# Kernel tuning notes

Measured on AMD Instinct MI355X. Metric: run time of the kernel, lower is better.

## Reference

```python
import jax, jax.numpy as jnp
import numpy as np

N_HEAD = 16
N_EMBD = 2048


def _rope(x):
    # x: (B, H, L, D). FAITHFUL to source: _apply_rope unpacks (B, L, H, D) on a
    # (B, H, L, D) tensor, so rotation angle = head_index * inv_freq, broadcast over
    # all sequence positions (a latent bug in the original, reproduced exactly).
    B, H, L, D = x.shape
    inv_freq = 1.0 / (10000.0 ** (jnp.arange(0, D, 2, dtype=jnp.float32) / D))  # (D/2,)
    theta = jnp.arange(H, dtype=jnp.float32)[:, None] * inv_freq[None, :]       # (H, D/2)
    cos = jnp.cos(theta)[None, :, None, :]  # (1, H, 1, D/2)
    sin = jnp.sin(theta)[None, :, None, :]
    xp = x.astype(jnp.float32).reshape(B, H, L, D // 2, 2)
    x0, x1 = xp[..., 0], xp[..., 1]
    r0 = x0 * cos - x1 * sin
    r1 = x0 * sin + x1 * cos
    return jnp.stack([r0, r1], axis=-1).reshape(B, H, L, D).astype(x.dtype)


def setup_inputs() -> dict:
    key = jax.random.key(0)
    k1, k2, k3 = jax.random.split(key, 3)
    B, L, C = 2, 2048, N_EMBD
    s = 1.0 / np.sqrt(C).astype(np.float32)
    x = jax.random.normal(k1, (B, L, C), dtype=jnp.float32)
    w_attn = jax.random.normal(k2, (3 * C, C), dtype=jnp.float32) * s
    w_proj = jax.random.normal(k3, (C, C), dtype=jnp.float32) * s
    return {"x": x, "w_attn": w_attn, "w_proj": w_proj}


def reference(x, w_attn, w_proj):
    B, L, C = x.shape
    H = N_HEAD
    D = C // H
    qkv = x @ w_attn.T                       # (B, L, 3C)
    q, k, v = jnp.split(qkv, 3, axis=2)
    q = q.reshape(B, L, H, D).transpose(0, 2, 1, 3)  # (B, H, L, D)
    k = k.reshape(B, L, H, D).transpose(0, 2, 1, 3)
    v = v.reshape(B, L, H, D).transpose(0, 2, 1, 3)
    q = _rope(q)
    k = _rope(k)
    attn = jnp.einsum('bhqd,bhkd->bhqk', q, k) * (1.0 / np.sqrt(D).astype(np.float32))
    causal = jnp.tril(jnp.ones((L, L), dtype=bool))
    attn = jnp.where(causal[None, None], attn, -jnp.inf)
    attn = jax.nn.softmax(attn, axis=-1)
    y = jnp.einsum('bhqk,bhkd->bhqd', attn, v)
    y = y.transpose(0, 2, 1, 3).reshape(B, L, C)
    return y @ w_proj.T
```

## Files before the change

kernel.cpp:

```cpp
#include <hip/hip_runtime.h>

typedef __attribute__((ext_vector_type(8))) short bf16x8;
typedef __attribute__((ext_vector_type(4))) float f32x4;

__device__ __forceinline__ unsigned short f2bf(float f) {
  unsigned int u = __float_as_uint(f);
  u += 0x7FFF + ((u >> 16) & 1);
  return (unsigned short)(u >> 16);
}

__device__ __forceinline__ void gload_lds16(const void* g, void* l) {
  __builtin_amdgcn_global_load_lds(
      (const __attribute__((address_space(1))) unsigned int*)g,
      (__attribute__((address_space(3))) unsigned int*)l,
      16, 0, 0);
}

#define MF(a, b, c) __builtin_amdgcn_mfma_f32_16x16x32_bf16((a), (b), (c), 0, 0, 0)
#define FENCE asm volatile("" ::: "memory")

__global__ void cast_f32_to_bf16(const float* __restrict__ in,
                                 unsigned short* __restrict__ out, int n4) {
  int stride = gridDim.x * blockDim.x;
  for (int i = blockIdx.x * blockDim.x + threadIdx.x; i < n4; i += stride) {
    float4 v = ((const float4*)in)[i];
    ushort4 o;
    o.x = f2bf(v.x); o.y = f2bf(v.y); o.z = f2bf(v.z); o.w = f2bf(v.w);
    ((ushort4*)out)[i] = o;
  }
}

template<int EPI>
__global__ __launch_bounds__(512, 2)
void gemm8p(const unsigned short* __restrict__ A,
            const unsigned short* __restrict__ Bw,
            float* __restrict__ Cf,
            unsigned short* __restrict__ Qo,
            unsigned short* __restrict__ Ko,
            unsigned short* __restrict__ Vo,
            int M, int N, int K, int Lseq) {
  __shared__ unsigned short lds[2][2][2][8192];
  const int tid = threadIdx.x;
  const int lane = tid & 63, w = tid >> 6;
  const int wm = w >> 2, wn = w & 3;
  const int bh = wn >> 1;
  const int bcol = (wn & 1) * 64;
  const int g4 = lane >> 4, r16 = lane & 15;
  const long arow0 = (long)blockIdx.y * 256;
  const long brow0 = (long)blockIdx.x * 256;

#define LDA(db, mf, kk)                                                       \
  (*(const bf16x8*)((const char*)&lds[0][db][wm][0] +                         \
                    (((mf)*16 + r16) << 7) +                                  \
                    ((((kk)*4 + g4) ^ (r16 & 7)) << 4)))
#define LDB(db, nf, kk)                                                       \
  (*(const bf16x8*)((const char*)&lds[1][db][bh][0] +                         \
                    ((bcol + (nf)*16 + r16) << 7) +                           \
                    ((((kk)*4 + g4) ^ (r16 & 7)) << 4)))

#define STG(mat, db, half, kt)                                                \
  do {                                                                        \
    const unsigned short* g_ = (mat) ? Bw : A;                                \
    long r0_ = ((mat) ? brow0 : arow0) + (half)*128;                          \
    int k0_ = (kt) << 6;                                                      \
    _Pragma("unroll")                                                         \
    for (int c_ = 0; c_ < 2; ++c_) {                                          \
      int off_ = (c_ << 13) + (tid << 4);                                     \
      int row_ = off_ >> 7;                                                   \
      int scb_ = ((off_ >> 4) & 7) ^ (row_ & 7);                              \
      gload_lds16(g_ + (r0_ + row_) * (long)K + k0_ + scb_ * 8,               \
                  (char*)&lds[mat][db][half][0] + off_);                      \
    }                                                                         \
  } while (0)

  f32x4 acc[8][4];
#pragma unroll
  for (int i = 0; i < 8; ++i)
#pragma unroll
    for (int j = 0; j < 4; ++j) acc[i][j] = (f32x4){0.f, 0.f, 0.f, 0.f};

  bf16x8 b00, b01, b10, b11, b20, b21, b30, b31;

#define PH(db, q, STAGE_STMT, VMSTMT)                                         \
  do {                                                                        \
    bf16x8 a00 = LDA(db, 2*(q), 0), a01 = LDA(db, 2*(q), 1);                  \
    bf16x8 a10 = LDA(db, 2*(q)+1, 0), a11 = LDA(db, 2*(q)+1, 1);              \
    STAGE_STMT;                                                               \
    VMSTMT;                                                                   \
    FENCE; __builtin_amdgcn_s_barrier(); FENCE;                               \
    __builtin_amdgcn_s_setprio(1);                                            \
    acc[2*(q)][0] = MF(a00, b00, acc[2*(q)][0]);                              \
    acc[2*(q)][0] = MF(a01, b01, acc[2*(q)][0]);                              \
    acc[2*(q)][1] = MF(a00, b10, acc[2*(q)][1]);                              \
    acc[2*(q)][1] = MF(a01, b11, acc[2*(q)][1]);                              \
    acc[2*(q)][2] = MF(a00, b20, acc[2*(q)][2]);                              \
    acc[2*(q)][2] = MF(a01, b21, acc[2*(q)][2]);                              \
    acc[2*(q)][3] = MF(a00, b30, acc[2*(q)][3]);                              \
    acc[2*(q)][3] = MF(a01, b31, acc[2*(q)][3]);                              \
    acc[2*(q)+1][0] = MF(a10, b00, acc[2*(q)+1][0]);                          \
    acc[2*(q)+1][0] = MF(a11, b01, acc[2*(q)+1][0]);                          \
    acc[2*(q)+1][1] = MF(a10, b10, acc[2*(q)+1][1]);                          \
    acc[2*(q)+1][1] = MF(a11, b11, acc[2*(q)+1][1]);                          \
    acc[2*(q)+1][2] = MF(a10, b20, acc[2*(q)+1][2]);                          \
    acc[2*(q)+1][2] = MF(a11, b21, acc[2*(q)+1][2]);                          \
    acc[2*(q)+1][3] = MF(a10, b30, acc[2*(q)+1][3]);                          \
    acc[2*(q)+1][3] = MF(a11, b31, acc[2*(q)+1][3]);                          \
    __builtin_amdgcn_s_setprio(0);                                            \
    FENCE; __builtin_amdgcn_s_barrier(); FENCE;                               \
  } while (0)

#define LOADB(db)                                                             \
  do {                                                                        \
    b00 = LDB(db, 0, 0); b01 = LDB(db, 0, 1);                                 \
    b10 = LDB(db, 1, 0); b11 = LDB(db, 1, 1);                                 \
    b20 = LDB(db, 2, 0); b21 = LDB(db, 2, 1);                                 \
    b30 = LDB(db, 3, 0); b31 = LDB(db, 3, 1);                                 \
  } while (0)

#define VM4 asm volatile("s_waitcnt vmcnt(4)" ::: "memory")

  const int NT = K >> 6;
  STG(0, 0, 0, 0); STG(0, 0, 1, 0);
  STG(1, 0, 0, 0); STG(1, 0, 1, 0);
  STG(1, 1, 0, 1); STG(1, 1, 1, 1);
  VM4;
  FENCE; __builtin_amdgcn_s_barrier(); FENCE;

  for (int i = 0; i < (NT >> 1); ++i) {
    const int t1 = 2 * i + 1;
    int n0 = 2 * i + 2; if (n0 > NT - 1) n0 = NT - 1;
    int n1 = 2 * i + 3; if (n1 > NT - 1) n1 = NT - 1;
    LOADB(0);
    PH(0, 0, STG(0, 1, 0, t1), );
    PH(0, 1, STG(0, 1, 1, t1), );
    PH(0, 2, STG(1, 0, 0, n0), );
    PH(0, 3, STG(1, 0, 1, n0), VM4);
    LOADB(1);
    PH(1, 0, STG(0, 0, 0, n0), );
    PH(1, 1, STG(0, 0, 1, n0), );
    PH(1, 2, STG(1, 1, 0, n1), );
    PH(1, 3, STG(1, 1, 1, n1), VM4);
  }
  asm volatile("s_waitcnt vmcnt(0)" ::: "memory");

  const float qscale = 0.08838834764831845f;
#pragma unroll
  for (int mf = 0; mf < 8; ++mf) {
#pragma unroll
    for (int nf = 0; nf < 4; ++nf) {
#pragma unroll
      for (int i = 0; i < 4; ++i) {
        long row = arow0 + wm * 128 + mf * 16 + 4 * g4 + i;
        long col = brow0 + wn * 64 + nf * 16 + r16;
        float v = acc[mf][nf][i];
        if (EPI == 0) {
          Cf[row * N + col] = v;
        } else {
          int which = (int)(col >> 11);
          int h = ((int)col >> 7) & 15;
          int d = (int)col & 127;
          int b = (int)(row >> 11);
          int l = (int)row & 2047;
          long bhead = (long)(b * 16 + h);
          if (which == 0)
            Qo[(bhead * Lseq + l) * 128 + d] = f2bf(v * qscale);
          else if (which == 1)
            Ko[(bhead * Lseq + l) * 128 + d] = f2bf(v);
          else
            Vo[(bhead * 128 + d) * Lseq + l] = f2bf(v);
        }
      }
    }
  }
#undef LDA
#undef LDB
#undef STG
#undef PH
#undef LOADB
#undef VM4
}

template<int EPI>
__global__ __launch_bounds__(256, 4)
void gemm_bt(const unsigned short* __restrict__ A,
             const unsigned short* __restrict__ Bw,
             float* __restrict__ Cf,
             unsigned short* __restrict__ Qo,
             unsigned short* __restrict__ Ko,
             unsigned short* __restrict__ Vo,
             int M, int N, int K, int Lseq, int nbx) {
  __shared__ unsigned short As[2][128 * 32];
  __shared__ unsigned short Bs[2][128 * 32];
  const int tid = threadIdx.x;
  const int lane = tid & 63, w = tid >> 6;
  const int wm = w >> 1, wn = w & 1;
  const int g4 = lane >> 4, r16 = lane & 15;

  const int nwg = gridDim.x;
  const int cpx = nwg >> 3;
  const int bid = (blockIdx.x & 7) * cpx + (blockIdx.x >> 3);
  const long arow0 = (long)(bid / nbx) * 128;
  const long brow0 = (long)(bid % nbx) * 128;

#define STAGE_G(k0_, buf_)                                                    \
  do {                                                                        \
    _Pragma("unroll")                                                         \
    for (int c_ = 0; c_ < 2; ++c_) {                                          \
      int off_ = (w << 11) + (c_ << 10) + (lane << 4);                        \
      int row_ = off_ >> 6;                                                   \
      int cbs_ = ((off_ >> 4) & 3) ^ ((row_ >> 1) & 3);                       \
      gload_lds16(A + (arow0 + row_) * (long)K + (k0_) + cbs_ * 8,            \
                  (char*)As[buf_] + off_);                                    \
      gload_lds16(Bw + (brow0 + row_) * (long)K + (k0_) + cbs_ * 8,           \
                  (char*)Bs[buf_] + off_);                                    \
    }                                                                         \
  } while (0)

  f32x4 acc[4][4];
#pragma unroll
  for (int i = 0; i < 4; ++i)
#pragma unroll
    for (int j = 0; j < 4; ++j) acc[i][j] = (f32x4){0.f, 0.f, 0.f, 0.f};

  const int T = K >> 5;
  int cur = 0;
  STAGE_G(0, 0);

  for (int t = 0; t < T; ++t) {
    if (t < T - 1) {
      STAGE_G((t + 1) << 5, cur ^ 1);
      asm volatile("s_waitcnt vmcnt(4)" ::: "memory");
    } else {
      asm volatile("s_waitcnt vmcnt(0)" ::: "memory");
    }
    __builtin_amdgcn_s_barrier();

    const int rb = g4 ^ ((r16 >> 1) & 3);
    bf16x8 af[4], bf[4];
#pragma unroll
    for (int mf = 0; mf < 4; ++mf)
      af[mf] = *(const bf16x8*)((const char*)As[cur] +
                                ((64 * wm + 16 * mf + r16) << 6) + (rb << 4));
#pragma unroll
    for (int nf = 0; nf < 4; ++nf)
      bf[nf] = *(const bf16x8*)((const char*)Bs[cur] +
                                ((64 * wn + 16 * nf + r16) << 6) + (rb << 4));
#pragma unroll
    for (int mf = 0; mf < 4; ++mf)
#pragma unroll
      for (int nf = 0; nf < 4; ++nf)
        acc[mf][nf] = MF(af[mf], bf[nf], acc[mf][nf]);
    asm volatile("" ::: "memory");
    __builtin_amdgcn_s_barrier();
    cur ^= 1;
  }
#undef STAGE_G

  const float qscale = 0.08838834764831845f;
#pragma unroll
  for (int mf = 0; mf < 4; ++mf) {
#pragma unroll
    for (int nf = 0; nf < 4; ++nf) {
#pragma unroll
      for (int i = 0; i < 4; ++i) {
        long row = arow0 + 64 * wm + 16 * mf + 4 * g4 + i;
        long col = brow0 + 64 * wn + 16 * nf + r16;
        float v = acc[mf][nf][i];
        if (EPI == 0) {
          Cf[row * N + col] = v;
        } else {
          int which = (int)(col >> 11);
          int h = ((int)col >> 7) & 15;
          int d = (int)col & 127;
          int b = (int)(row >> 11);
          int l = (int)row & 2047;
          long bhead = (long)(b * 16 + h);
          if (which == 0)
            Qo[(bhead * Lseq + l) * 128 + d] = f2bf(v * qscale);
          else if (which == 1)
            Ko[(bhead * Lseq + l) * 128 + d] = f2bf(v);
          else
            Vo[(bhead * 128 + d) * Lseq + l] = f2bf(v);
        }
      }
    }
  }
}

__global__ __launch_bounds__(256, 2)
void attn_fwd(const unsigned short* __restrict__ Q,
              const unsigned short* __restrict__ K,
              const unsigned short* __restrict__ Vt,
              unsigned short* __restrict__ Y, int L) {
  const int D = 128;
  const int id = blockIdx.x;
  const int g = id & 7, kk = id >> 3;
  const int bh = (g << 2) + (kk >> 5);
  const int qt = 31 - (kk & 31);
  const int tid = threadIdx.x, lane = tid & 63, w = tid >> 6;
  const int g4 = lane >> 4, r16 = lane & 15;
  const int q0 = qt * 64;

  __shared__ unsigned short Klds[2 * 64 * 128];
  __shared__ unsigned short Vlds[2 * 128 * 64];
  __shared__ unsigned short P[4][16][72];

  const unsigned short* Qh = Q + (long)bh * L * D;
  const unsigned short* Kh = K + (long)bh * L * D;
  const unsigned short* Vh = Vt + (long)bh * D * L;

#define STAGE_TILE(kt_, buf_)                                                 \
  do {                                                                        \
    const int kbase_ = (kt_) * 64;                                            \
    _Pragma("unroll")                                                         \
    for (int r_ = 0; r_ < 4; ++r_) {                                          \
      int off_ = (tid << 4) + (r_ << 12);                                     \
      int krow_ = off_ >> 8, kcb_ = (off_ >> 4) & 15;                         \
      int kcbs_ = kcb_ ^ (krow_ & 7);                                         \
      gload_lds16(Kh + (long)(kbase_ + krow_) * 128 + kcbs_ * 8,              \
                  (char*)Klds + (buf_)*16384 + (w << 10) + (r_ << 12));       \
      int vrow_ = off_ >> 7, vcb_ = (off_ >> 4) & 7;                          \
      int vcbs_ = vcb_ ^ (vrow_ & 7);                                         \
      gload_lds16(Vh + (long)vrow_ * L + kbase_ + vcbs_ * 8,                  \
                  (char*)Vlds + (buf_)*16384 + (w << 10) + (r_ << 12));       \
    }                                                                         \
  } while (0)

  bf16x8 qf[4];
  {
    long qrow = q0 + 16 * w + r16;
#pragma unroll
    for (int ks = 0; ks < 4; ++ks)
      qf[ks] = *(const bf16x8*)(Qh + qrow * D + ks * 32 + g4 * 8);
  }
  f32x4 o[8];
#pragma unroll
  for (int j = 0; j < 8; ++j) o[j] = (f32x4){0.f, 0.f, 0.f, 0.f};
  float mrun[4] = {-1e30f, -1e30f, -1e30f, -1e30f};
  float lrun[4] = {0.f, 0.f, 0.f, 0.f};

  int cur = 0;
  STAGE_TILE(0, 0);

  for (int kt = 0; kt <= qt; ++kt) {
    if (kt < qt) {
      STAGE_TILE(kt + 1, cur ^ 1);
      asm volatile("s_waitcnt vmcnt(8)" ::: "memory");
    } else {
      asm volatile("s_waitcnt vmcnt(0)" ::: "memory");
    }
    __builtin_amdgcn_s_barrier();

    const char* Kl = (const char*)Klds + cur * 16384;
    const char* Vl = (const char*)Vlds + cur * 16384;

    f32x4 s[4];
#pragma unroll
    for (int nf = 0; nf < 4; ++nf) s[nf] = (f32x4){0.f, 0.f, 0.f, 0.f};
#pragma unroll
    for (int ks = 0; ks < 4; ++ks) {
#pragma unroll
      for (int nf = 0; nf < 4; ++nf) {
        int row = 16 * nf + r16;
        bf16x8 kf = *(const bf16x8*)(Kl + row * 256 +
                                     (((ks * 4 + g4) ^ (row & 7)) << 4));
        s[nf] = MF(qf[ks], kf, s[nf]);
      }
    }

    const bool diag = (kt == qt);
#pragma unroll
    for (int i = 0; i < 4; ++i) {
      int qg = q0 + 16 * w + 4 * g4 + i;
      float sv[4];
      float rmax = -1e30f;
#pragma unroll
      for (int nf = 0; nf < 4; ++nf) {
        float t = s[nf][i];
        if (diag && (kt * 64 + 16 * nf + r16) > qg) t = -1e30f;
        sv[nf] = t;
        rmax = fmaxf(rmax, t);
      }
      rmax = fmaxf(rmax, __shfl_xor(rmax, 1));
      rmax = fmaxf(rmax, __shfl_xor(rmax, 2));
      rmax = fmaxf(rmax, __shfl_xor(rmax, 4));
      rmax = fmaxf(rmax, __shfl_xor(rmax, 8));
      float mnew = fmaxf(mrun[i], rmax);
      float corr = __expf(mrun[i] - mnew);
      mrun[i] = mnew;
      float rs = 0.f;
#pragma unroll
      for (int nf = 0; nf < 4; ++nf) {
        float pv = __expf(sv[nf] - mnew);
        P[w][4 * g4 + i][16 * nf + r16] = f2bf(pv);
        rs += pv;
      }
      rs += __shfl_xor(rs, 1);
      rs += __shfl_xor(rs, 2);
      rs += __shfl_xor(rs, 4);
      rs += __shfl_xor(rs, 8);
      lrun[i] = lrun[i] * corr + rs;
#pragma unroll
      for (int nf2 = 0; nf2 < 8; ++nf2) o[nf2][i] *= corr;
    }
#pragma unroll
    for (int ks2 = 0; ks2 < 2; ++ks2) {
      bf16x8 pf = *(const bf16x8*)(&P[w][r16][ks2 * 32 + g4 * 8]);
#pragma unroll
      for (int nf2 = 0; nf2 < 8; ++nf2) {
        int row = 16 * nf2 + r16;
        bf16x8 vf = *(const bf16x8*)(Vl + row * 128 +
                                     (((ks2 * 4 + g4) ^ (row & 7)) << 4));
        o[nf2] = MF(pf, vf, o[nf2]);
      }
    }
    asm volatile("" ::: "memory");
    __builtin_amdgcn_s_barrier();
    cur ^= 1;
  }
#undef STAGE_TILE

  const int b = bh >> 4, h = bh & 15;
#pragma unroll
  for (int nf2 = 0; nf2 < 8; ++nf2) {
#pragma unroll
    for (int i = 0; i < 4; ++i) {
      long row = (long)b * L + q0 + 16 * w + 4 * g4 + i;
      float v = o[nf2][i] / lrun[i];
      Y[row * 2048 + h * 128 + 16 * nf2 + r16] = f2bf(v);
    }
  }
}

extern "C" void kernel_launch(void* const* d_in, const int* in_sizes, int n_in,
                              void* d_out, int out_size, void* d_ws,
                              size_t ws_size, hipStream_t stream) {
  const float* x = (const float*)d_in[0];
  const float* wa = (const float*)d_in[1];
  const float* wp = (const float*)d_in[2];
  float* out = (float*)d_out;
  const int B = 2, L = 2048, C = 2048;
  const int M = B * L;

  unsigned short* xb = (unsigned short*)d_ws;
  unsigned short* wab = xb + (size_t)M * C;
  unsigned short* wpb = wab + (size_t)3 * C * C;
  unsigned short* Qb = wpb + (size_t)C * C;
  unsigned short* Kb = Qb + (size_t)M * C;
  unsigned short* Vb = Kb + (size_t)M * C;
  unsigned short* Yb = Vb + (size_t)M * C;

  cast_f32_to_bf16<<<2048, 256, 0, stream>>>(x, xb, M * C / 4);
  cast_f32_to_bf16<<<2048, 256, 0, stream>>>(wa, wab, 3 * C * C / 4);
  cast_f32_to_bf16<<<1024, 256, 0, stream>>>(wp, wpb, C * C / 4);

  gemm8p<1><<<dim3(3 * C / 256, M / 256), 512, 0, stream>>>(
      xb, wab, nullptr, Qb, Kb, Vb, M, 3 * C, C, L);

  attn_fwd<<<1024, 256, 0, stream>>>(Qb, Kb, Vb, Yb, L);

  gemm_bt<0><<<(M / 128) * (C / 128), 256, 0, stream>>>(
      Yb, wpb, out, nullptr, nullptr, nullptr, M, C, C, L, C / 128);
}
```

Before: 332.8 us.

## Software-pipeline A-fragment LDS reads and swizzle block order in QKV GEMM

Restructures the QKV projection GEMM main loop so the A fragments for the next compute phase are read from LDS into registers (double-buffered aaA/aaB) while the current phase's MFMAs run. This removes one barrier per phase, cutting from two to one. It also changes the launch to a 1D grid of 384 blocks with a remapping that groups blocks sharing the same B (weight) tiles, aiming for better L2 reuse. The cost is more register pressure from the extra fragment buffers, and a reordered global-to-LDS staging schedule with vmcnt(2) waits that must stay race-free.

```diff
diff --git a/kernel.cpp b/kernel.cpp
--- a/kernel.cpp
+++ b/kernel.cpp
@@ -18,6 +18,7 @@
 
 #define MF(a, b, c) __builtin_amdgcn_mfma_f32_16x16x32_bf16((a), (b), (c), 0, 0, 0)
 #define FENCE asm volatile("" ::: "memory")
+#define BARF do { FENCE; __builtin_amdgcn_s_barrier(); FENCE; } while (0)
 
 __global__ void cast_f32_to_bf16(const float* __restrict__ in,
                                  unsigned short* __restrict__ out, int n4) {
@@ -39,74 +40,59 @@
             unsigned short* __restrict__ Ko,
             unsigned short* __restrict__ Vo,
             int M, int N, int K, int Lseq) {
-  __shared__ unsigned short lds[2][2][2][8192];
+  __shared__ unsigned short Al[2][2][8192];
+  __shared__ unsigned short Bl[2][2][8192];
   const int tid = threadIdx.x;
   const int lane = tid & 63, w = tid >> 6;
   const int wm = w >> 2, wn = w & 3;
   const int bh = wn >> 1;
   const int bcol = (wn & 1) * 64;
   const int g4 = lane >> 4, r16 = lane & 15;
-  const long arow0 = (long)blockIdx.y * 256;
-  const long brow0 = (long)blockIdx.x * 256;
+
+  const int swz = (blockIdx.x & 7) * 48 + (blockIdx.x >> 3);
+  const int bx = swz >> 4, by = swz & 15;
+  const long arow0 = (long)by * 256;
+  const long brow0 = (long)bx * 256;
 
 #define LDA(db, mf, kk)                                                       \
-  (*(const bf16x8*)((const char*)&lds[0][db][wm][0] +                         \
-                    (((mf)*16 + r16) << 7) +                                  \
+  (*(const bf16x8*)((const char*)&Al[db][wm][0] + (((mf)*16 + r16) << 7) +    \
                     ((((kk)*4 + g4) ^ (r16 & 7)) << 4)))
 #define LDB(db, nf, kk)                                                       \
-  (*(const bf16x8*)((const char*)&lds[1][db][bh][0] +                         \
+  (*(const bf16x8*)((const char*)&Bl[db][bh][0] +                             \
                     ((bcol + (nf)*16 + r16) << 7) +                           \
                     ((((kk)*4 + g4) ^ (r16 & 7)) << 4)))
 
-#define STG(mat, db, half, kt)                                                \
-  do {                                                                        \
-    const unsigned short* g_ = (mat) ? Bw : A;                                \
-    long r0_ = ((mat) ? brow0 : arow0) + (half)*128;                          \
+#define STGA(db, half, kt)                                                    \
+  do {                                                                        \
+    long r0_ = arow0 + (half)*128;                                            \
     int k0_ = (kt) << 6;                                                      \
     _Pragma("unroll")                                                         \
     for (int c_ = 0; c_ < 2; ++c_) {                                          \
       int off_ = (c_ << 13) + (tid << 4);                                     \
       int row_ = off_ >> 7;                                                   \
       int scb_ = ((off_ >> 4) & 7) ^ (row_ & 7);                              \
-      gload_lds16(g_ + (r0_ + row_) * (long)K + k0_ + scb_ * 8,               \
-                  (char*)&lds[mat][db][half][0] + off_);                      \
+      gload_lds16(A + (r0_ + row_) * (long)K + k0_ + scb_ * 8,                \
+                  (char*)&Al[db][half][0] + off_);                            \
     }                                                                         \
   } while (0)
-
-  f32x4 acc[8][4];
-#pragma unroll
-  for (int i = 0; i < 8; ++i)
-#pragma unroll
-    for (int j = 0; j < 4; ++j) acc[i][j] = (f32x4){0.f, 0.f, 0.f, 0.f};
-
-  bf16x8 b00, b01, b10, b11, b20, b21, b30, b31;
-
-#define PH(db, q, STAGE_STMT, VMSTMT)                                         \
-  do {                                                                        \
-    bf16x8 a00 = LDA(db, 2*(q), 0), a01 = LDA(db, 2*(q), 1);                  \
-    bf16x8 a10 = LDA(db, 2*(q)+1, 0), a11 = LDA(db, 2*(q)+1, 1);              \
-    STAGE_STMT;                                                               \
-    VMSTMT;                                                                   \
-    FENCE; __builtin_amdgcn_s_barrier(); FENCE;                               \
-    __builtin_amdgcn_s_setprio(1);                                            \
-    acc[2*(q)][0] = MF(a00, b00, acc[2*(q)][0]);                              \
-    acc[2*(q)][0] = MF(a01, b01, acc[2*(q)][0]);                              \
-    acc[2*(q)][1] = MF(a00, b10, acc[2*(q)][1]);                              \
-    acc[2*(q)][1] = MF(a01, b11, acc[2*(q)][1]);                              \
-    acc[2*(q)][2] = MF(a00, b20, acc[2*(q)][2]);                              \
-    acc[2*(q)][2] = MF(a01, b21, acc[2*(q)][2]);                              \
-    acc[2*(q)][3] = MF(a00, b30, acc[2*(q)][3]);                              \
-    acc[2*(q)][3] = MF(a01, b31, acc[2*(q)][3]);                              \
-    acc[2*(q)+1][0] = MF(a10, b00, acc[2*(q)+1][0]);                          \
-    acc[2*(q)+1][0] = MF(a11, b01, acc[2*(q)+1][0]);                          \
-    acc[2*(q)+1][1] = MF(a10, b10, acc[2*(q)+1][1]);                          \
-    acc[2*(q)+1][1] = MF(a11, b11, acc[2*(q)+1][1]);                          \
-    acc[2*(q)+1][2] = MF(a10, b20, acc[2*(q)+1][2]);                          \
-    acc[2*(q)+1][2] = MF(a11, b21, acc[2*(q)+1][2]);                          \
-    acc[2*(q)+1][3] = MF(a10, b30, acc[2*(q)+1][3]);                          \
-    acc[2*(q)+1][3] = MF(a11, b31, acc[2*(q)+1][3]);                          \
-    __builtin_amdgcn_s_setprio(0);                                            \
-    FENCE; __builtin_amdgcn_s_barrier(); FENCE;                               \
+#define STGB(db, half, kt)                                                    \
+  do {                                                                        \
+    long r0_ = brow0 + (half)*128;                                            \
+    int k0_ = (kt) << 6;                                                      \
+    _Pragma("unroll")                                                         \
+    for (int c_ = 0; c_ < 2; ++c_) {                                          \
+      int off_ = (c_ << 13) + (tid << 4);                                     \
+      int row_ = off_ >> 7;                                                   \
+      int scb_ = ((off_ >> 4) & 7) ^ (row_ & 7);                              \
+      gload_lds16(Bw + (r0_ + row_) * (long)K + k0_ + scb_ * 8,               \
+                  (char*)&Bl[db][half][0] + off_);                            \
+    }                                                                         \
+  } while (0)
+
+#define PREF(dst, db, q)                                                      \
+  do {                                                                        \
+    dst[0] = LDA(db, 2*(q), 0);   dst[1] = LDA(db, 2*(q), 1);                 \
+    dst[2] = LDA(db, 2*(q)+1, 0); dst[3] = LDA(db, 2*(q)+1, 1);               \
   } while (0)
 
 #define LOADB(db)                                                             \
@@ -117,29 +103,67 @@
     b30 = LDB(db, 3, 0); b31 = LDB(db, 3, 1);                                 \
   } while (0)
 
-#define VM4 asm volatile("s_waitcnt vmcnt(4)" ::: "memory")
+#define CMP(src, q)                                                           \
+  do {                                                                        \
+    __builtin_amdgcn_s_setprio(1);                                            \
+    acc[2*(q)][0]   = MF(src[0], b00, acc[2*(q)][0]);                         \
+    acc[2*(q)][0]   = MF(src[1], b01, acc[2*(q)][0]);                         \
+    acc[2*(q)][1]   = MF(src[0], b10, acc[2*(q)][1]);                         \
+    acc[2*(q)][1]   = MF(src[1], b11, acc[2*(q)][1]);                         \
+    acc[2*(q)][2]   = MF(src[0], b20, acc[2*(q)][2]);                         \
+    acc[2*(q)][2]   = MF(src[1], b21, acc[2*(q)][2]);                         \
+    acc[2*(q)][3]   = MF(src[0], b30, acc[2*(q)][3]);                         \
+    acc[2*(q)][3]   = MF(src[1], b31, acc[2*(q)][3]);                         \
+    acc[2*(q)+1][0] = MF(src[2], b00, acc[2*(q)+1][0]);                       \
+    acc[2*(q)+1][0] = MF(src[3], b01, acc[2*(q)+1][0]);                       \
+    acc[2*(q)+1][1] = MF(src[2], b10, acc[2*(q)+1][1]);                       \
+    acc[2*(q)+1][1] = MF(src[3], b11, acc[2*(q)+1][1]);                       \
+    acc[2*(q)+1][2] = MF(src[2], b20, acc[2*(q)+1][2]);                       \
+    acc[2*(q)+1][2] = MF(src[3], b21, acc[2*(q)+1][2]);                       \
+    acc[2*(q)+1][3] = MF(src[2], b30, acc[2*(q)+1][3]);                       \
+    acc[2*(q)+1][3] = MF(src[3], b31, acc[2*(q)+1][3]);                       \
+    __builtin_amdgcn_s_setprio(0);                                            \
+  } while (0)
+
+#define VM2 asm volatile("s_waitcnt vmcnt(2)" ::: "memory")
+
+  f32x4 acc[8][4];
+#pragma unroll
+  for (int i = 0; i < 8; ++i)
+#pragma unroll
+    for (int j = 0; j < 4; ++j) acc[i][j] = (f32x4){0.f, 0.f, 0.f, 0.f};
+
+  bf16x8 aaA[4], aaB[4];
+  bf16x8 b00, b01, b10, b11, b20, b21, b30, b31;
 
   const int NT = K >> 6;
-  STG(0, 0, 0, 0); STG(0, 0, 1, 0);
-  STG(1, 0, 0, 0); STG(1, 0, 1, 0);
-  STG(1, 1, 0, 1); STG(1, 1, 1, 1);
-  VM4;
-  FENCE; __builtin_amdgcn_s_barrier(); FENCE;
+  STGA(0, 0, 0); STGA(0, 1, 0);
+  STGB(0, 0, 0); STGB(0, 1, 0);
+  STGB(1, 0, 1); STGB(1, 1, 1);
+  asm volatile("s_waitcnt vmcnt(0)" ::: "memory");
+  BARF;
+  PREF(aaA, 0, 0);
 
   for (int i = 0; i < (NT >> 1); ++i) {
     const int t1 = 2 * i + 1;
-    int n0 = 2 * i + 2; if (n0 > NT - 1) n0 = NT - 1;
-    int n1 = 2 * i + 3; if (n1 > NT - 1) n1 = NT - 1;
-    LOADB(0);
-    PH(0, 0, STG(0, 1, 0, t1), );
-    PH(0, 1, STG(0, 1, 1, t1), );
-    PH(0, 2, STG(1, 0, 0, n0), );
-    PH(0, 3, STG(1, 0, 1, n0), VM4);
-    LOADB(1);
-    PH(1, 0, STG(0, 0, 0, n0), );
-    PH(1, 1, STG(0, 0, 1, n0), );
-    PH(1, 2, STG(1, 1, 0, n1), );
-    PH(1, 3, STG(1, 1, 1, n1), VM4);
+    int t2 = 2 * i + 2; if (t2 > NT - 1) t2 = NT - 1;
+    int t3 = 2 * i + 3; if (t3 > NT - 1) t3 = NT - 1;
+    LOADB(0); PREF(aaB, 0, 1); STGA(1, 0, t1);
+    CMP(aaA, 0); BARF;
+    PREF(aaA, 0, 2); STGA(1, 1, t1);
+    CMP(aaB, 1); BARF;
+    PREF(aaB, 0, 3); STGB(0, 0, t2); VM2;
+    CMP(aaA, 2); BARF;
+    PREF(aaA, 1, 0); STGB(0, 1, t2);
+    CMP(aaB, 3); BARF;
+    LOADB(1); PREF(aaB, 1, 1); STGA(0, 0, t2);
+    CMP(aaA, 0); BARF;
+    PREF(aaA, 1, 2); STGA(0, 1, t2); STGB(1, 0, t3);
+    CMP(aaB, 1); BARF;
+    PREF(aaB, 1, 3); STGB(1, 1, t3); VM2;
+    CMP(aaA, 2); BARF;
+    PREF(aaA, 0, 0);
+    CMP(aaB, 3); BARF;
   }
   asm volatile("s_waitcnt vmcnt(0)" ::: "memory");
 
@@ -174,10 +198,12 @@
   }
 #undef LDA
 #undef LDB
-#undef STG
-#undef PH
+#undef STGA
+#undef STGB
+#undef PREF
 #undef LOADB
-#undef VM4
+#undef CMP
+#undef VM2
 }
 
 template<int EPI>
@@ -454,8 +480,8 @@
   cast_f32_to_bf16<<<2048, 256, 0, stream>>>(wa, wab, 3 * C * C / 4);
   cast_f32_to_bf16<<<1024, 256, 0, stream>>>(wp, wpb, C * C / 4);
 
-  gemm8p<1><<<dim3(3 * C / 256, M / 256), 512, 0, stream>>>(
-      xb, wab, nullptr, Qb, Kb, Vb, M, 3 * C, C, L);
+  gemm8p<1><<<384, 512, 0, stream>>>(xb, wab, nullptr, Qb, Kb, Vb,
+                                     M, 3 * C, C, L);
 
   attn_fwd<<<1024, 256, 0, stream>>>(Qb, Kb, Vb, Yb, L);
 
```

After: 412.5 us. +23.9%, slower.
